# Kernel optimization log

Measured on AMD Instinct MI355X. Metric: run time of the kernel, lower is better.

## Reference

```python
import jax, jax.numpy as jnp
import numpy as np

N = 131072
N_SIGMAS = 64
SEG = N // N_SIGMAS  # 2048, also the gaussian window size


def setup_inputs() -> dict:
    key = jax.random.key(0)
    ks = jax.random.split(key, 4)
    n, h = 256, 256
    x = jax.random.normal(ks[0], (n,), dtype=jnp.float32)
    W1 = jax.random.normal(ks[1], (n, h), dtype=jnp.float32) / jnp.sqrt(jnp.float32(n))
    b1 = jnp.zeros((h,), dtype=jnp.float32)
    W2 = jax.random.normal(ks[2], (h, N_SIGMAS), dtype=jnp.float32) / jnp.sqrt(jnp.float32(h))
    b2 = jnp.zeros((N_SIGMAS,), dtype=jnp.float32)
    W3 = jax.random.normal(ks[3], (n, N), dtype=jnp.float32) / jnp.sqrt(jnp.float32(n))
    b3 = jnp.zeros((N,), dtype=jnp.float32)
    return {"x": x, "W1": W1, "b1": b1, "W2": W2, "b2": b2, "W3": W3, "b3": b3}


def _gaussian_windows(sigmas):
    # gaussian_kernel(window_size=SEG, sigma) vmapped over sigmas -> (n_sigmas, SEG)
    mu = SEG / 2.0
    t = jnp.arange(SEG, dtype=sigmas.dtype)
    w = jnp.exp(-((t[None, :] - mu) ** 2) / (2.0 * sigmas[:, None] ** 2))
    return w / jnp.sum(w, axis=1, keepdims=True)


def reference(x, W1, b1, W2, b2, W3, b3):
    # sigma-predictor MLP: Dense -> swish -> Dense
    s = jax.nn.swish(jnp.dot(x, W1) + b1)
    sigmas = jnp.dot(s, W2) + b2              # (n_sigmas,)
    y = jnp.dot(x, W3) + b3                   # (N,)
    windows = _gaussian_windows(sigmas)       # (n_sigmas, SEG)
    segs = y.reshape(N_SIGMAS, SEG)           # equal split, N divisible by n_sigmas
    out = jax.vmap(lambda a, w: jnp.convolve(a, w, mode="same"))(segs, windows)
    return out.reshape(-1)                    # hstack of segments
```

## Files before the change

kernel.cpp:

```cpp
#include <hip/hip_runtime.h>
#include <math.h>

#define NTOT 131072
#define NSIG 64
#define SEGL 2048
#define NIN 256


__global__ __launch_bounds__(256) void k_y(
    const float* __restrict__ x,  const float* __restrict__ W1,
    const float* __restrict__ b1, const float* __restrict__ W2,
    const float* __restrict__ b2, const float* __restrict__ W3,
    const float* __restrict__ b3, float* __restrict__ y,
    float* __restrict__ w_all, int* __restrict__ Dv)
{
  __shared__ float xl[NIN];
  __shared__ float sl[256];
  __shared__ float red[4];
  __shared__ float bc[2];

  const int t = threadIdx.x;
  const int bx0 = (int)blockIdx.x;
  const int bx = ((bx0 & 7) << 6) | (bx0 >> 3);
  const int col = (bx << 8) + t;

  xl[t] = x[t];
  __syncthreads();

  const float* p = W3 + col;
  float a = b3[col];

  if (bx0 < NSIG) {
    float am = b1[t];
    #pragma unroll 16
    for (int n = 0; n < NIN; ++n) {
      const float xv = xl[n];
      a  = fmaf(xv, p[(size_t)n * NTOT], a);
      am = fmaf(xv, W1[n * 256 + t], am);
    }
    y[col] = a;
    sl[t] = am / (1.0f + expf(-am));
    __syncthreads();

    const int seg = bx0;
    float v = sl[t] * W2[t * NSIG + seg];
    #pragma unroll
    for (int o = 32; o > 0; o >>= 1) v += __shfl_down(v, o, 64);
    const int lane = t & 63, wid = t >> 6;
    if (lane == 0) red[wid] = v;
    __syncthreads();
    if (t == 0) bc[0] = red[0] + red[1] + red[2] + red[3] + b2[seg];
    __syncthreads();
    const float sig = bc[0];

    const float inv2 = 1.0f / (2.0f * sig * sig);
    const float Df = 12.0f * fabsf(sig) + 4.0f;
    const int D = (Df >= 1024.0f) ? 1024 : (int)Df;
    const int dlo = -D;
    const int dhi = (D < 1023) ? D : 1023;
    const int cnt = dhi - dlo + 1;

    float zp = 0.0f;
    for (int i = t; i < cnt; i += 256) {
      const float d = (float)(dlo + i);
      const float e = expf(-d * d * inv2);
      w_all[seg * SEGL + 1024 + dlo + i] = e;
      zp += e;
    }
    v = zp;
    #pragma unroll
    for (int o = 32; o > 0; o >>= 1) v += __shfl_down(v, o, 64);
    if (lane == 0) red[wid] = v;
    __syncthreads();
    if (t == 0) bc[1] = red[0] + red[1] + red[2] + red[3];
    __syncthreads();
    const float iZ = 1.0f / bc[1];
    for (int i = t; i < cnt; i += 256)
      w_all[seg * SEGL + 1024 + dlo + i] *= iZ;
    if (t == 0) Dv[seg] = D;
  } else {
    #pragma unroll 16
    for (int n = 0; n < NIN; ++n)
      a = fmaf(xl[n], p[(size_t)n * NTOT], a);
    y[col] = a;
  }
}

__global__ __launch_bounds__(256) void k_conv(
    const float* __restrict__ y, const float* __restrict__ w_all,
    const int* __restrict__ Dv, float* __restrict__ out)
{
  __shared__ float S[2560];
  __shared__ float Wl[SEGL];

  const int t = threadIdx.x;
  const int bx0 = (int)blockIdx.x;
  const int bx = ((bx0 & 7) << 6) | (bx0 >> 3);
  const int seg = bx >> 3;
  const int M0 = (bx & 7) << 8;
  const int sbase = M0 - 1026;

  const int D = Dv[seg];
  const int dlo = -D;
  const int dhi = (D < 1023) ? D : 1023;
  const int cnt = dhi - dlo + 1;

  for (int i = t; i < cnt; i += 256)
    Wl[1024 + dlo + i] = w_all[seg * SEGL + 1024 + dlo + i];

  #pragma unroll
  for (int j = 0; j < 10; ++j) {
    const int i = t + j * 256;
    const int g = sbase + i;
    S[i] = (g >= 0 && g < SEGL) ? y[seg * SEGL + g] : 0.0f;
  }
  __syncthreads();

  float a = 0.0f;
  for (int d = dlo; d <= dhi; ++d)
    a = fmaf(Wl[1024 + d], S[t + 1025 - d], a);
  out[seg * SEGL + M0 + t] = a;
}

extern "C" void kernel_launch(void* const* d_in, const int* in_sizes, int n_in,
                              void* d_out, int out_size, void* d_ws, size_t ws_size,
                              hipStream_t stream) {
  const float* x  = (const float*)d_in[0];
  const float* W1 = (const float*)d_in[1];
  const float* b1 = (const float*)d_in[2];
  const float* W2 = (const float*)d_in[3];
  const float* b2 = (const float*)d_in[4];
  const float* W3 = (const float*)d_in[5];
  const float* b3 = (const float*)d_in[6];
  float* out = (float*)d_out;

  char* ws = (char*)d_ws;
  float* y     = (float*)(ws);
  float* w_all = (float*)(ws + 524288);
  int*   Dv    = (int*)  (ws + 1048576);

  hipLaunchKernelGGL(k_y, dim3(512), dim3(256), 0, stream,
                     x, W1, b1, W2, b2, W3, b3, y, w_all, Dv);
  hipLaunchKernelGGL(k_conv, dim3(512), dim3(256), 0, stream,
                     y, w_all, Dv, out);
}
```

Baseline: 31.83 us.

## Fuse projection and convolution into one cooperative kernel with grid sync

Merges the y-projection/sigma kernel and the convolution kernel into a single cooperative launch, separated by a grid-wide barrier, so the second kernel launch and its gap go away. It also limits the staging load of y into shared memory to the range the gaussian support actually reaches, instead of always loading 10 chunks. The cost is a grid sync, higher shared memory per block, and the requirement that all 512 blocks be co-resident. The launch-bounds hint is set to 2 blocks per SM.

```diff
diff --git a/kernel.cpp b/kernel.cpp
--- a/kernel.cpp
+++ b/kernel.cpp
@@ -1,23 +1,28 @@
 #include <hip/hip_runtime.h>
+#include <hip/hip_cooperative_groups.h>
 #include <math.h>
+
+namespace cg = cooperative_groups;
 
 #define NTOT 131072
 #define NSIG 64
 #define SEGL 2048
 #define NIN 256
 
-
-__global__ __launch_bounds__(256) void k_y(
+__global__ __launch_bounds__(256, 2) void k_all(
     const float* __restrict__ x,  const float* __restrict__ W1,
     const float* __restrict__ b1, const float* __restrict__ W2,
     const float* __restrict__ b2, const float* __restrict__ W3,
     const float* __restrict__ b3, float* __restrict__ y,
-    float* __restrict__ w_all, int* __restrict__ Dv)
+    float* __restrict__ w_all, int* __restrict__ Dv,
+    float* __restrict__ out)
 {
   __shared__ float xl[NIN];
   __shared__ float sl[256];
   __shared__ float red[4];
   __shared__ float bc[2];
+  __shared__ float S[2560];
+  __shared__ float Wl[SEGL];
 
   const int t = threadIdx.x;
   const int bx0 = (int)blockIdx.x;
@@ -84,18 +89,9 @@
       a = fmaf(xl[n], p[(size_t)n * NTOT], a);
     y[col] = a;
   }
-}
 
-__global__ __launch_bounds__(256) void k_conv(
-    const float* __restrict__ y, const float* __restrict__ w_all,
-    const int* __restrict__ Dv, float* __restrict__ out)
-{
-  __shared__ float S[2560];
-  __shared__ float Wl[SEGL];
+  cg::this_grid().sync();
 
-  const int t = threadIdx.x;
-  const int bx0 = (int)blockIdx.x;
-  const int bx = ((bx0 & 7) << 6) | (bx0 >> 3);
   const int seg = bx >> 3;
   const int M0 = (bx & 7) << 8;
   const int sbase = M0 - 1026;
@@ -108,18 +104,18 @@
   for (int i = t; i < cnt; i += 256)
     Wl[1024 + dlo + i] = w_all[seg * SEGL + 1024 + dlo + i];
 
-  #pragma unroll
-  for (int j = 0; j < 10; ++j) {
-    const int i = t + j * 256;
+  const int ilo = 1025 - dhi;
+  const int ihi = 1281 + D;
+  for (int i = ilo + t; i < ihi; i += 256) {
     const int g = sbase + i;
     S[i] = (g >= 0 && g < SEGL) ? y[seg * SEGL + g] : 0.0f;
   }
   __syncthreads();
 
-  float a = 0.0f;
+  float acc = 0.0f;
   for (int d = dlo; d <= dhi; ++d)
-    a = fmaf(Wl[1024 + d], S[t + 1025 - d], a);
-  out[seg * SEGL + M0 + t] = a;
+    acc = fmaf(Wl[1024 + d], S[t + 1025 - d], acc);
+  out[seg * SEGL + M0 + t] = acc;
 }
 
 extern "C" void kernel_launch(void* const* d_in, const int* in_sizes, int n_in,
@@ -139,8 +135,8 @@
   float* w_all = (float*)(ws + 524288);
   int*   Dv    = (int*)  (ws + 1048576);
 
-  hipLaunchKernelGGL(k_y, dim3(512), dim3(256), 0, stream,
-                     x, W1, b1, W2, b2, W3, b3, y, w_all, Dv);
-  hipLaunchKernelGGL(k_conv, dim3(512), dim3(256), 0, stream,
-                     y, w_all, Dv, out);
+  void* args[] = {(void*)&x, (void*)&W1, (void*)&b1, (void*)&W2, (void*)&b2,
+                  (void*)&W3, (void*)&b3, (void*)&y, (void*)&w_all, (void*)&Dv,
+                  (void*)&out};
+  hipLaunchCooperativeKernel((void*)k_all, dim3(512), dim3(256), args, 0, stream);
 }
```

After: 109.4 us. 3.44x slower.

## Split GEMV reduction across wavefronts with float4 loads and shared-memory partial sums

Applied to the files above, without the earlier changes.

The y=xW3 GEMV (and the W1 MLP GEMV) now splits the 256-long K dimension across the four wavefronts of each block. Each thread loads float4 of four adjacent columns instead of one scalar column, and partial sums are combined through shared memory. This raises the number of independent memory requests in flight per thread and shortens each thread's serial dependency chain from 256 to 64 iterations. It costs 8 KB of extra shared memory and an added barrier plus reduction step.

```diff
diff --git a/kernel.cpp b/kernel.cpp
--- a/kernel.cpp
+++ b/kernel.cpp
@@ -15,6 +15,8 @@
     float* __restrict__ w_all, int* __restrict__ Dv)
 {
   __shared__ float xl[NIN];
+  __shared__ float party[1024];
+  __shared__ float partm[1024];
   __shared__ float sl[256];
   __shared__ float red[4];
   __shared__ float bc[2];
@@ -22,68 +24,89 @@
   const int t = threadIdx.x;
   const int bx0 = (int)blockIdx.x;
   const int bx = ((bx0 & 7) << 6) | (bx0 >> 3);
-  const int col = (bx << 8) + t;
+  const int colbase = bx << 8;
+  const int g = t >> 6;
+  const int q = (t & 63) << 2;
 
   xl[t] = x[t];
   __syncthreads();
 
-  const float* p = W3 + col;
-  float a = b3[col];
+  const float* wp = W3 + (size_t)(g << 6) * NTOT + colbase + q;
+  float4 a = make_float4(0.0f, 0.0f, 0.0f, 0.0f);
 
   if (bx0 < NSIG) {
-    float am = b1[t];
-    #pragma unroll 16
-    for (int n = 0; n < NIN; ++n) {
-      const float xv = xl[n];
-      a  = fmaf(xv, p[(size_t)n * NTOT], a);
-      am = fmaf(xv, W1[n * 256 + t], am);
+    const float* mp = W1 + (g << 6) * 256 + q;
+    float4 am = make_float4(0.0f, 0.0f, 0.0f, 0.0f);
+    #pragma unroll 8
+    for (int k = 0; k < 64; ++k) {
+      const float xv = xl[(g << 6) + k];
+      const float4 wv = *reinterpret_cast<const float4*>(wp + (size_t)k * NTOT);
+      const float4 mv = *reinterpret_cast<const float4*>(mp + k * 256);
+      a.x  = fmaf(xv, wv.x, a.x);  a.y  = fmaf(xv, wv.y, a.y);
+      a.z  = fmaf(xv, wv.z, a.z);  a.w  = fmaf(xv, wv.w, a.w);
+      am.x = fmaf(xv, mv.x, am.x); am.y = fmaf(xv, mv.y, am.y);
+      am.z = fmaf(xv, mv.z, am.z); am.w = fmaf(xv, mv.w, am.w);
     }
-    y[col] = a;
-    sl[t] = am / (1.0f + expf(-am));
-    __syncthreads();
-
-    const int seg = bx0;
-    float v = sl[t] * W2[t * NSIG + seg];
-    #pragma unroll
-    for (int o = 32; o > 0; o >>= 1) v += __shfl_down(v, o, 64);
-    const int lane = t & 63, wid = t >> 6;
-    if (lane == 0) red[wid] = v;
-    __syncthreads();
-    if (t == 0) bc[0] = red[0] + red[1] + red[2] + red[3] + b2[seg];
-    __syncthreads();
-    const float sig = bc[0];
-
-    const float inv2 = 1.0f / (2.0f * sig * sig);
-    const float Df = 12.0f * fabsf(sig) + 4.0f;
-    const int D = (Df >= 1024.0f) ? 1024 : (int)Df;
-    const int dlo = -D;
-    const int dhi = (D < 1023) ? D : 1023;
-    const int cnt = dhi - dlo + 1;
-
-    float zp = 0.0f;
-    for (int i = t; i < cnt; i += 256) {
-      const float d = (float)(dlo + i);
-      const float e = expf(-d * d * inv2);
-      w_all[seg * SEGL + 1024 + dlo + i] = e;
-      zp += e;
-    }
-    v = zp;
-    #pragma unroll
-    for (int o = 32; o > 0; o >>= 1) v += __shfl_down(v, o, 64);
-    if (lane == 0) red[wid] = v;
-    __syncthreads();
-    if (t == 0) bc[1] = red[0] + red[1] + red[2] + red[3];
-    __syncthreads();
-    const float iZ = 1.0f / bc[1];
-    for (int i = t; i < cnt; i += 256)
-      w_all[seg * SEGL + 1024 + dlo + i] *= iZ;
-    if (t == 0) Dv[seg] = D;
+    *reinterpret_cast<float4*>(&party[(g << 8) + q]) = a;
+    *reinterpret_cast<float4*>(&partm[(g << 8) + q]) = am;
   } else {
     #pragma unroll 16
-    for (int n = 0; n < NIN; ++n)
-      a = fmaf(xl[n], p[(size_t)n * NTOT], a);
-    y[col] = a;
+    for (int k = 0; k < 64; ++k) {
+      const float xv = xl[(g << 6) + k];
+      const float4 wv = *reinterpret_cast<const float4*>(wp + (size_t)k * NTOT);
+      a.x = fmaf(xv, wv.x, a.x);  a.y = fmaf(xv, wv.y, a.y);
+      a.z = fmaf(xv, wv.z, a.z);  a.w = fmaf(xv, wv.w, a.w);
+    }
+    *reinterpret_cast<float4*>(&party[(g << 8) + q]) = a;
   }
+  __syncthreads();
+
+  y[colbase + t] = party[t] + party[256 + t] + party[512 + t] + party[768 + t]
+                   + b3[colbase + t];
+
+  if (bx0 >= NSIG) return;
+
+  const float amf = partm[t] + partm[256 + t] + partm[512 + t] + partm[768 + t]
+                    + b1[t];
+  sl[t] = amf / (1.0f + expf(-amf));
+  __syncthreads();
+
+  const int seg = bx0;
+  float v = sl[t] * W2[t * NSIG + seg];
+  #pragma unroll
+  for (int o = 32; o > 0; o >>= 1) v += __shfl_down(v, o, 64);
+  const int lane = t & 63, wid = t >> 6;
+  if (lane == 0) red[wid] = v;
+  __syncthreads();
+  if (t == 0) bc[0] = red[0] + red[1] + red[2] + red[3] + b2[seg];
+  __syncthreads();
+  const float sig = bc[0];
+
+  const float inv2 = 1.0f / (2.0f * sig * sig);
+  const float Df = 12.0f * fabsf(sig) + 4.0f;
+  const int D = (Df >= 1024.0f) ? 1024 : (int)Df;
+  const int dlo = -D;
+  const int dhi = (D < 1023) ? D : 1023;
+  const int cnt = dhi - dlo + 1;
+
+  float zp = 0.0f;
+  for (int i = t; i < cnt; i += 256) {
+    const float d = (float)(dlo + i);
+    const float e = expf(-d * d * inv2);
+    w_all[seg * SEGL + 1024 + dlo + i] = e;
+    zp += e;
+  }
+  v = zp;
+  #pragma unroll
+  for (int o = 32; o > 0; o >>= 1) v += __shfl_down(v, o, 64);
+  if (lane == 0) red[wid] = v;
+  __syncthreads();
+  if (t == 0) bc[1] = red[0] + red[1] + red[2] + red[3];
+  __syncthreads();
+  const float iZ = 1.0f / bc[1];
+  for (int i = t; i < cnt; i += 256)
+    w_all[seg * SEGL + 1024 + dlo + i] *= iZ;
+  if (t == 0) Dv[seg] = D;
 }
 
 __global__ __launch_bounds__(256) void k_conv(
@@ -111,8 +134,8 @@
   #pragma unroll
   for (int j = 0; j < 10; ++j) {
     const int i = t + j * 256;
-    const int g = sbase + i;
-    S[i] = (g >= 0 && g < SEGL) ? y[seg * SEGL + g] : 0.0f;
+    const int gg = sbase + i;
+    S[i] = (gg >= 0 && gg < SEGL) ? y[seg * SEGL + gg] : 0.0f;
   }
   __syncthreads();
 
```

New measurement: 35.89 us. 1.13x slower.
